# Kernel tuning notes

Measured on AMD Instinct MI355X. Metric: run time of the kernel, lower is better.

The kernel has to match this reference:

```python
import jax, jax.numpy as jnp
import numpy as np

B, T, M, H = 256, 64, 256, 256


def setup_inputs() -> dict:
    key = jax.random.key(0)
    ks = jax.random.split(key, 16)
    n = jax.random.normal
    s = 0.05  # small init so tanh/sigmoid stay in sane range
    return {
        "enc_inputs": n(ks[0], (T, B, M), jnp.float32),  # module transposes (0,1) itself
        "y": n(ks[1], (B, T, 1), jnp.float32),
        "W_d": n(ks[2], (M, 2 * H), jnp.float32) * s,
        "b_Wd": n(ks[3], (M,), jnp.float32) * s,
        "U_d": n(ks[4], (M, M), jnp.float32) * s,
        "v_d": n(ks[5], (1, M), jnp.float32) * s,
        "w_tilda": n(ks[6], (1, M + 1), jnp.float32) * s,
        "b_wt": n(ks[7], (1,), jnp.float32) * s,
        "W_ih": n(ks[8], (4 * H, 1), jnp.float32) * s,
        "W_hh": n(ks[9], (4 * H, H), jnp.float32) * s,
        "b_ih": n(ks[10], (4 * H,), jnp.float32) * s,
        "b_hh": n(ks[11], (4 * H,), jnp.float32) * s,
        "W_y": n(ks[12], (H, H + M), jnp.float32) * s,
        "b_Wy": n(ks[13], (H,), jnp.float32) * s,
        "v_y": n(ks[14], (1, H), jnp.float32) * s,
        "b_vy": n(ks[15], (1,), jnp.float32) * s,
    }


def reference(enc_inputs, y, W_d, b_Wd, U_d, v_d, w_tilda, b_wt,
              W_ih, W_hh, b_ih, b_hh, W_y, b_Wy, v_y, b_vy):
    enc = jnp.swapaxes(enc_inputs, 0, 1)                 # (B,T,M)
    # U_d(enc) is loop-invariant; hoist (same math as recomputing per step)
    y1 = jnp.einsum('btm,nm->btn', enc, U_d)             # (B,T,M)
    ys = jnp.swapaxes(y, 0, 1)                           # (T,B,1) scanned over time
    b = enc.shape[0]
    d0 = jnp.zeros((b, H), enc.dtype)
    s0 = jnp.zeros((b, H), enc.dtype)
    c0 = jnp.zeros((b, M), enc.dtype)

    def step(carry, y_t):
        d, sp, _ = carry
        # Bahdanau-style temporal attention over encoder steps
        x1 = jnp.concatenate([d, sp], axis=1) @ W_d.T + b_Wd      # (B,M)
        l = jnp.tanh(x1[:, None, :] + y1) @ v_d[0]                # (B,T)
        beta = jax.nn.softmax(l, axis=1)
        c = jnp.einsum('bt,btm->bm', beta, enc)                   # (B,M)
        # scalar driving input for the decoder LSTM cell
        y_til = jnp.concatenate([c, y_t], axis=1) @ w_tilda.T + b_wt  # (B,1)
        # torch.nn.LSTMCell update with (h, c) = (d, sp)
        gates = y_til @ W_ih.T + b_ih + d @ W_hh.T + b_hh         # (B,4H)
        i, f, g, o = jnp.split(gates, 4, axis=1)
        sp_new = jax.nn.sigmoid(f) * sp + jax.nn.sigmoid(i) * jnp.tanh(g)
        d_new = jax.nn.sigmoid(o) * jnp.tanh(sp_new)
        return (d_new, sp_new, c), None

    (d, sp, c), _ = jax.lax.scan(step, (d0, s0, c0), ys)
    h = jnp.concatenate([d, c], axis=1) @ W_y.T + b_Wy            # (B,H)
    return h @ v_y.T + b_vy                                        # (B,1)
```

## Files before the change

### kernel.cpp

```cpp
#include <hip/hip_runtime.h>


#define Bx 256
#define Tx 64
#define Mx 256
#define Hx 256
#define NT 1024
#define XS 20

typedef unsigned int  uint;
typedef unsigned short ushort;
typedef _Float16 h2  __attribute__((ext_vector_type(2)));
typedef float    f2v __attribute__((ext_vector_type(2)));

__device__ __forceinline__ float4 ld4(const float* p) { return *(const float4*)p; }
__device__ __forceinline__ float h2f(ushort s) {
  union { ushort s; _Float16 h; } c; c.s = s; return (float)c.h;
}
__device__ __forceinline__ ushort f2h(float f) {
  union { _Float16 h; ushort s; } c; c.h = (_Float16)f; return c.s;
}
__device__ __forceinline__ uint pk2(float a, float b) {
  return (uint)f2h(a) | ((uint)f2h(b) << 16);
}

#if defined(__has_builtin)
#if __has_builtin(__builtin_amdgcn_rcpf)
#define RCPF(x) __builtin_amdgcn_rcpf(x)
#endif
#if __has_builtin(__builtin_amdgcn_fdot2)
#define HAVE_FDOT2 1
#endif
#if __has_builtin(__builtin_amdgcn_cvt_pk_f32_fp8) && __has_builtin(__builtin_amdgcn_cvt_pk_fp8_f32)
#define HAVE_FP8 1
#endif
#endif
#ifndef RCPF
#define RCPF(x) (1.0f / (x))
#endif

__device__ __forceinline__ float tanh_fast(float x) {
  float e2 = __expf(2.0f * x);
  return 1.0f - 2.0f * RCPF(e2 + 1.0f);
}
__device__ __forceinline__ float tanh_pre(float z2) {
  return 1.0f - 2.0f * RCPF(__expf(z2) + 1.0f);
}
__device__ __forceinline__ float sigm(float x) {
  return RCPF(1.0f + __expf(-x));
}
__device__ __forceinline__ float wave_sum(float v) {
  #pragma unroll
  for (int o = 1; o < 64; o <<= 1) v += __shfl_xor(v, o, 64);
  return v;
}
__device__ __forceinline__ int xsw(int m) { return (m >> 4) * XS + (m & 15); }

__device__ __forceinline__ uint sw8(float f) {
  union { float f; uint u; } c; c.f = f;
  uint s = (c.u >> 31) << 7;
  float a = fabsf(f);
  if (!(a >= 0.0009765625f)) return s;
  if (a >= 448.f) return s | 0x7e;
  int e = (int)((c.u >> 23) & 0xff) - 127;
  if (e < -6) { int q = (int)(a * 512.f + 0.5f); return s | (uint)q; }
  uint m = ((c.u & 0x7fffff) + 0x80000) >> 20;
  if (m == 8) { m = 0; ++e; }
  if (e > 8) return s | 0x7e;
  return s | ((uint)(e + 7) << 3) | m;
}
__device__ __forceinline__ float sw8d(uint b) {
  uint s = b >> 7, e = (b >> 3) & 0xf, m = b & 7;
  float v;
  if (e) { union { uint u; float f; } c; c.u = ((e + 120u) << 23) | (m << 20); v = c.f; }
  else v = (float)m * 0.001953125f;
  return s ? -v : v;
}
__device__ __forceinline__ uint pk_fp8x4(float w0, float w1, float w2, float w3) {
#ifdef HAVE_FP8
  int u = 0;
  u = __builtin_amdgcn_cvt_pk_fp8_f32(w0, w1, u, false);
  u = __builtin_amdgcn_cvt_pk_fp8_f32(w2, w3, u, true);
  return (uint)u;
#else
  return sw8(w0) | (sw8(w1) << 8) | (sw8(w2) << 16) | (sw8(w3) << 24);
#endif
}
template <bool HI>
__device__ __forceinline__ f2v dec2(uint w) {
#ifdef HAVE_FP8
  return __builtin_amdgcn_cvt_pk_f32_fp8((int)w, HI);
#else
  uint b0 = HI ? ((w >> 16) & 0xffu) : (w & 0xffu);
  uint b1 = HI ? (w >> 24) : ((w >> 8) & 0xffu);
  return f2v{sw8d(b0), sw8d(b1)};
#endif
}
__device__ __forceinline__ f2v dotq(uint w, float4 a, f2v acc) {
  acc += dec2<false>(w) * f2v{a.x, a.y};
  acc += dec2<true>(w)  * f2v{a.z, a.w};
  return acc;
}

__global__ __launch_bounds__(256)
void pack_weights(const float* __restrict__ W_d,
                  const float* __restrict__ W_hh,
                  const float* __restrict__ U_d,
                  const float* __restrict__ W_y,
                  uint4* __restrict__ Whh8q,
                  uint4* __restrict__ Wd8q,
                  uint4* __restrict__ Ud8,
                  float* __restrict__ Wyt) {
  const int blk = blockIdx.x, tid = threadIdx.x;
  if (blk < 16) {
    const int k16 = blk;
    #pragma unroll
    for (int q = 0; q < 4; ++q) {
      const int j = tid + 256 * q;
      const float* wr = W_hh + (size_t)j * 256 + 16 * k16;
      float4 a = ld4(wr), b = ld4(wr + 4), c = ld4(wr + 8), d = ld4(wr + 12);
      uint4 u;
      u.x = pk_fp8x4(16.f * a.x, 16.f * a.y, 16.f * a.z, 16.f * a.w);
      u.y = pk_fp8x4(16.f * b.x, 16.f * b.y, 16.f * b.z, 16.f * b.w);
      u.z = pk_fp8x4(16.f * c.x, 16.f * c.y, 16.f * c.z, 16.f * c.w);
      u.w = pk_fp8x4(16.f * d.x, 16.f * d.y, 16.f * d.z, 16.f * d.w);
      Whh8q[k16 * 1024 + j] = u;
    }
  } else if (blk < 48) {
    const int k16 = blk - 16;
    const float* wr = W_d + (size_t)tid * 512 + 16 * k16;
    float4 a = ld4(wr), b = ld4(wr + 4), c = ld4(wr + 8), d = ld4(wr + 12);
    uint4 u;
    u.x = pk_fp8x4(16.f * a.x, 16.f * a.y, 16.f * a.z, 16.f * a.w);
    u.y = pk_fp8x4(16.f * b.x, 16.f * b.y, 16.f * b.z, 16.f * b.w);
    u.z = pk_fp8x4(16.f * c.x, 16.f * c.y, 16.f * c.z, 16.f * c.w);
    u.w = pk_fp8x4(16.f * d.x, 16.f * d.y, 16.f * d.z, 16.f * d.w);
    Wd8q[k16 * 256 + tid] = u;
  } else if (blk < 80) {
    const int m8 = blk - 48;
    float4 a = ld4(U_d + (size_t)tid * 256 + 8 * m8);
    float4 b = ld4(U_d + (size_t)tid * 256 + 8 * m8 + 4);
    Ud8[m8 * 256 + tid] = uint4{pk2(2.f * a.x, 2.f * a.y), pk2(2.f * a.z, 2.f * a.w),
                                pk2(2.f * b.x, 2.f * b.y), pk2(2.f * b.z, 2.f * b.w)};
  } else {
    const int k0 = (blk - 80) * 4;
    float4 w = ld4(W_y + (size_t)tid * 512 + k0);
    Wyt[(k0 + 0) * 256 + tid] = w.x;
    Wyt[(k0 + 1) * 256 + tid] = w.y;
    Wyt[(k0 + 2) * 256 + tid] = w.z;
    Wyt[(k0 + 3) * 256 + tid] = w.w;
  }
}

__global__ __launch_bounds__(NT, 1)
void fused(const float* __restrict__ enc,
           const float* __restrict__ yv,
           const float* __restrict__ b_Wd,
           const float* __restrict__ v_d,
           const float* __restrict__ w_tilda,
           const float* __restrict__ b_wt,
           const float* __restrict__ W_ih,
           const float* __restrict__ b_ih,
           const float* __restrict__ b_hh,
           const float* __restrict__ b_Wy,
           const float* __restrict__ v_y,
           const float* __restrict__ b_vy,
           const uint4* __restrict__ Whh8q,
           const uint4* __restrict__ Wd8q,
           const uint4* __restrict__ Ud8,
           const float* __restrict__ Wyt,
           ushort* __restrict__ Y1,
           float* __restrict__ out)
{
  extern __shared__ __align__(16) uint4 dynls[];
  uint4* wdl = dynls;
  uint4* whl = dynls + 8192;
  __shared__ __align__(16) float dsp_s[2 * Hx];
  __shared__ __align__(16) float xq_s[2 * 16 * XS];
  __shared__ __align__(16) float vd_s[16 * XS];
  __shared__ float gates_s[1024];
  __shared__ float dcfin_s[2 * Hx];
  __shared__ float l_s[Tx];
  __shared__ uint  beta2_s[Tx / 2];
  __shared__ float e_s[Tx];
  __shared__ float red_s[4];
  __shared__ float ytil_s;
  __shared__ unsigned flagX, flagL, flagE;

  const int b   = blockIdx.x;
  const int tid = threadIdx.x;
  const int h   = tid & 255;
  const int p   = tid >> 8;
  const size_t BM = (size_t)Bx * Mx;

  #pragma unroll
  for (int i = 0; i < 8; ++i) wdl[i * NT + tid] = Wd8q[i * NT + tid];
  whl[tid] = Whh8q[15 * 1024 + tid];
  if (tid < 256) vd_s[xsw(tid)] = v_d[tid];
  if (tid < 512) dsp_s[tid] = 0.0f;
  if (tid == 0) { flagX = 0u; flagL = 0u; flagE = 0u; }

  float bj0 = 0.f, bj1 = 0.f;
  if (tid < 512) { bj0 = b_ih[tid] + b_hh[tid]; bj1 = b_ih[tid + 512] + b_hh[tid + 512]; }
  float bWd_r = 0.f;
  if (tid >= 512 && tid < 768) bWd_r = 2.0f * b_Wd[tid - 512];
  float wih0 = 0.f, wih1 = 0.f, wih2 = 0.f, wih3 = 0.f;
  if (tid < 256) {
    wih0 = W_ih[tid]; wih1 = W_ih[tid + 256]; wih2 = W_ih[tid + 512]; wih3 = W_ih[tid + 768];
  }
  float yv_r = 0.f;
  if (tid >= 512 && tid < 576) yv_r = yv[b * Tx + (tid - 512)];
  const float wty = w_tilda[Mx];
  const float bwt = b_wt[0];

  if (tid < Tx) {
    const float* er = enc + (size_t)tid * BM + (size_t)b * Mx;
    float acc = 0.0f;
    for (int m = 0; m < Mx; m += 4) {
      float4 e4 = ld4(er + m);
      float4 w4 = ld4(w_tilda + m);
      acc += e4.x * w4.x + e4.y * w4.y + e4.z * w4.z + e4.w * w4.w;
    }
    e_s[tid] = acc;
  }

  {
    const int n = h;
    const float* eb = enc + (size_t)b * Mx;
    for (int tb = p * 16; tb < p * 16 + 16; tb += 8) {
      f2v acc2[8];
      #pragma unroll
      for (int j = 0; j < 8; ++j) acc2[j] = f2v{0.f, 0.f};
      #pragma unroll 2
      for (int m8 = 0; m8 < 32; ++m8) {
        uint4 u = Ud8[m8 * 256 + n];
        f2v w01 = f2v{h2f((ushort)u.x), h2f((ushort)(u.x >> 16))};
        f2v w23 = f2v{h2f((ushort)u.y), h2f((ushort)(u.y >> 16))};
        f2v w45 = f2v{h2f((ushort)u.z), h2f((ushort)(u.z >> 16))};
        f2v w67 = f2v{h2f((ushort)u.w), h2f((ushort)(u.w >> 16))};
        #pragma unroll
        for (int j = 0; j < 8; ++j) {
          const float* ep = eb + (size_t)(tb + j) * BM + 8 * m8;
          float4 ea = ld4(ep), eb4 = ld4(ep + 4);
          acc2[j] += f2v{ea.x, ea.y} * w01;
          acc2[j] += f2v{ea.z, ea.w} * w23;
          acc2[j] += f2v{eb4.x, eb4.y} * w45;
          acc2[j] += f2v{eb4.z, eb4.w} * w67;
        }
      }
      #pragma unroll
      for (int j = 0; j < 8; ++j)
        Y1[((size_t)b * Tx + tb + j) * Mx + n] = f2h(acc2[j].x + acc2[j].y);
    }
  }
  __syncthreads();

  float e_r = 0.0f;
  if (tid >= 512 && tid < 576) e_r = e_s[tid - 512];

  float sp_reg = 0.0f;

  for (int t = 0; t < Tx; ++t) {
    float gi = 0.0f, gg = 0.0f;
    if (tid < 512) {
      f2v ga = f2v{0.f, 0.f}, gb = f2v{0.f, 0.f};
      const uint4* wp = Whh8q + tid;
      #pragma unroll 2
      for (int c = 0; c < 15; ++c) {
        uint4 wa = wp[c * 1024];
        uint4 wb = wp[c * 1024 + 512];
        const float4* ap = (const float4*)dsp_s + 4 * c;
        float4 a0 = ap[0], a1 = ap[1], a2 = ap[2], a3 = ap[3];
        ga = dotq(wa.x, a0, ga); ga = dotq(wa.y, a1, ga);
        ga = dotq(wa.z, a2, ga); ga = dotq(wa.w, a3, ga);
        gb = dotq(wb.x, a0, gb); gb = dotq(wb.y, a1, gb);
        gb = dotq(wb.z, a2, gb); gb = dotq(wb.w, a3, gb);
      }
      {
        uint4 wa = whl[tid];
        uint4 wb = whl[tid + 512];
        const float4* ap = (const float4*)dsp_s + 60;
        float4 a0 = ap[0], a1 = ap[1], a2 = ap[2], a3 = ap[3];
        ga = dotq(wa.x, a0, ga); ga = dotq(wa.y, a1, ga);
        ga = dotq(wa.z, a2, ga); ga = dotq(wa.w, a3, ga);
        gb = dotq(wb.x, a0, gb); gb = dotq(wb.y, a1, gb);
        gb = dotq(wb.z, a2, gb); gb = dotq(wb.w, a3, gb);
      }
      gi = (ga.x + ga.y) * 0.0625f + bj0;
      gg = (gb.x + gb.y) * 0.0625f + bj1;
      if (tid >= 256) {
        gates_s[tid]       = gi;
        gates_s[tid + 512] = gg;
        __threadfence_block();
        if ((tid & 63) == 0)
          __hip_atomic_fetch_add(&flagE, 1u, __ATOMIC_RELEASE, __HIP_MEMORY_SCOPE_WORKGROUP);
      }
    } else {
      const int idx = tid - 512;
      const int m = idx & 255, q = idx >> 8;
      const int tq = idx >> 3, lq = idx & 7;
      const ushort* y1r = Y1 + ((size_t)b * Tx + tq) * Mx + lq * 32;
      uint4 yq0 = *(const uint4*)(y1r);
      uint4 yq1 = *(const uint4*)(y1r + 8);
      uint4 yq2 = *(const uint4*)(y1r + 16);
      uint4 yq3 = *(const uint4*)(y1r + 24);
      {
        f2v xa2 = f2v{0.f, 0.f};
        const uint4* xp = wdl + m + (q * 16) * 256;
        #pragma unroll 4
        for (int i = 0; i < 16; ++i) {
          uint4 u = xp[i * 256];
          const float4* ap = (const float4*)dsp_s + 64 * q + 4 * i;
          float4 a0 = ap[0], a1 = ap[1], a2 = ap[2], a3 = ap[3];
          xa2 = dotq(u.x, a0, xa2); xa2 = dotq(u.y, a1, xa2);
          xa2 = dotq(u.z, a2, xa2); xa2 = dotq(u.w, a3, xa2);
        }
        xq_s[q * (16 * XS) + xsw(m)] = (xa2.x + xa2.y) * 0.125f
                                     + (q == 0 ? bWd_r : 0.0f);
      }
      __threadfence_block();
      if ((threadIdx.x & 63) == 0)
        __hip_atomic_fetch_add(&flagX, 1u, __ATOMIC_RELEASE, __HIP_MEMORY_SCOPE_WORKGROUP);
      const unsigned tgtX = 8u * (unsigned)(t + 1);
      while (__hip_atomic_load(&flagX, __ATOMIC_ACQUIRE, __HIP_MEMORY_SCOPE_WORKGROUP) < tgtX) {}

      {
        float ps = 0.0f;
        uint yy[8] = {yq0.x, yq0.y, yq0.z, yq0.w, yq1.x, yq1.y, yq1.z, yq1.w};
        uint zz[8] = {yq2.x, yq2.y, yq2.z, yq2.w, yq3.x, yq3.y, yq3.z, yq3.w};
        #pragma unroll
        for (int g = 0; g < 8; ++g) {
          const int c   = 2 * lq + (g >> 2);
          const int off = c * XS + 4 * (g & 3);
          float4 xa0 = *(const float4*)(xq_s + off);
          float4 xa1 = *(const float4*)(xq_s + 16 * XS + off);
          float4 vv  = *(const float4*)(vd_s + off);
          uint ya = (g < 4) ? yy[2 * g] : zz[2 * (g - 4)];
          uint yb = (g < 4) ? yy[2 * g + 1] : zz[2 * (g - 4) + 1];
          ps += tanh_pre(xa0.x + xa1.x + h2f((ushort)ya)) * vv.x
              + tanh_pre(xa0.y + xa1.y + h2f((ushort)(ya >> 16))) * vv.y
              + tanh_pre(xa0.z + xa1.z + h2f((ushort)yb)) * vv.z
              + tanh_pre(xa0.w + xa1.w + h2f((ushort)(yb >> 16))) * vv.w;
        }
        ps += __shfl_xor(ps, 1, 64);
        ps += __shfl_xor(ps, 2, 64);
        ps += __shfl_xor(ps, 4, 64);
        if (lq == 0) l_s[tq] = ps;
      }
      __threadfence_block();
      if ((threadIdx.x & 63) == 0)
        __hip_atomic_fetch_add(&flagL, 1u, __ATOMIC_RELEASE, __HIP_MEMORY_SCOPE_WORKGROUP);

      if (idx < 64) {
        __builtin_amdgcn_s_setprio(1);
        const unsigned tgtL = 8u * (unsigned)(t + 1);
        while (__hip_atomic_load(&flagL, __ATOMIC_ACQUIRE, __HIP_MEMORY_SCOPE_WORKGROUP) < tgtL) {}
        float e0  = __expf(l_s[idx]);
        float den = e0;
        float num = e0 * e_r;
        #pragma unroll
        for (int o = 1; o < 64; o <<= 1) {
          den += __shfl_xor(den, o, 64);
          num += __shfl_xor(num, o, 64);
        }
        if (t == Tx - 1) {
          float beta = e0 * RCPF(den);
          float bn = __shfl_xor(beta, 1, 64);
          if (!(idx & 1)) beta2_s[idx >> 1] = pk2(beta, bn);
        }
        if (idx == t) ytil_s = num * RCPF(den) + wty * yv_r + bwt;
        __threadfence_block();
        if (idx == 0)
          __hip_atomic_fetch_add(&flagE, 1u, __ATOMIC_RELEASE, __HIP_MEMORY_SCOPE_WORKGROUP);
        __builtin_amdgcn_s_setprio(0);
      }
    }

    if (tid < 256) {
      const unsigned tgtE = 5u * (unsigned)(t + 1);
      while (__hip_atomic_load(&flagE, __ATOMIC_ACQUIRE, __HIP_MEMORY_SCOPE_WORKGROUP) < tgtE) {}
      __builtin_amdgcn_s_setprio(1);
      const float ytil = ytil_s;
      float fi = sigm(gi                  + ytil * wih0);
      float ff = sigm(gates_s[256 + tid]  + ytil * wih1);
      float fg = tanh_fast(gg             + ytil * wih2);
      float fo = sigm(gates_s[768 + tid]  + ytil * wih3);
      float spn = ff * sp_reg + fi * fg;
      float dn  = fo * tanh_fast(spn);
      sp_reg = spn;
      dsp_s[tid]       = dn;
      dsp_s[256 + tid] = spn;
      if (t == Tx - 1) dcfin_s[tid] = dn;
      __builtin_amdgcn_s_setprio(0);
    }
    __syncthreads();
  }

  if (tid >= 512) {
    const int idx = tid - 512;
    const int m = idx >> 1, q = idx & 1;
    float acc = 0.0f;
    #pragma unroll 4
    for (int j = 0; j < 32; ++j) {
      const int tt = q * 32 + j;
      uint bp = beta2_s[tt >> 1];
      float bb = (tt & 1) ? h2f((ushort)(bp >> 16)) : h2f((ushort)bp);
      acc += bb * enc[(size_t)tt * BM + (size_t)b * Mx + m];
    }
    acc += __shfl_xor(acc, 1, 64);
    if (q == 0) dcfin_s[256 + m] = acc;
  }
  __syncthreads();

  {
    float a = 0.0f;
    const float* wy = Wyt + h;
    for (int k = 128 * p; k < 128 * p + 128; ++k)
      a += wy[(size_t)k * 256] * dcfin_s[k];
    gates_s[p * 256 + h] = a;
  }
  __syncthreads();
  if (tid < 256) {
    float aa = gates_s[h] + gates_s[256 + h] + gates_s[512 + h] + gates_s[768 + h]
             + b_Wy[h];
    float po = aa * v_y[h];
    po = wave_sum(po);
    if ((tid & 63) == 0) red_s[tid >> 6] = po;
  }
  __syncthreads();
  if (tid == 0) out[b] = red_s[0] + red_s[1] + red_s[2] + red_s[3] + b_vy[0];
}

extern "C" void kernel_launch(void* const* d_in, const int* in_sizes, int n_in,
                              void* d_out, int out_size, void* d_ws, size_t ws_size,
                              hipStream_t stream) {
  const float* enc     = (const float*)d_in[0];
  const float* yv      = (const float*)d_in[1];
  const float* W_d     = (const float*)d_in[2];
  const float* b_Wd    = (const float*)d_in[3];
  const float* U_d     = (const float*)d_in[4];
  const float* v_d     = (const float*)d_in[5];
  const float* w_tilda = (const float*)d_in[6];
  const float* b_wt    = (const float*)d_in[7];
  const float* W_ih    = (const float*)d_in[8];
  const float* W_hh    = (const float*)d_in[9];
  const float* b_ih    = (const float*)d_in[10];
  const float* b_hh    = (const float*)d_in[11];
  const float* W_y     = (const float*)d_in[12];
  const float* b_Wy    = (const float*)d_in[13];
  const float* v_y     = (const float*)d_in[14];
  const float* b_vy    = (const float*)d_in[15];
  float* outp = (float*)d_out;

  char* ws = (char*)d_ws;
  uint4* Whh8q = (uint4*)ws;
  uint4* Wd8q  = (uint4*)(ws + (256 << 10));
  uint4* Ud8   = (uint4*)(ws + (384 << 10));
  float* Wyt   = (float*)(ws + (512 << 10));
  ushort* Y1   = (ushort*)(ws + (1024 << 10));

  const int DYN_LDS = (128 + 16) << 10;
  hipFuncSetAttribute((const void*)fused,
                      hipFuncAttributeMaxDynamicSharedMemorySize, DYN_LDS);

  hipLaunchKernelGGL(pack_weights, dim3(208), dim3(256), 0, stream,
                     W_d, W_hh, U_d, W_y, Whh8q, Wd8q, Ud8, Wyt);
  hipLaunchKernelGGL(fused, dim3(Bx), dim3(NT), DYN_LDS, stream,
                     enc, yv, b_Wd, v_d, w_tilda, b_wt, W_ih, b_ih, b_hh,
                     b_Wy, v_y, b_vy, Whh8q, Wd8q, Ud8, Wyt, Y1, outp);
}
```

Measured before the change: 598.2 us.

## Redistribute attention and LSTM gate work across all 1024 threads per step

Each timestep's work is now split across all 16 waves instead of being partitioned into LSTM-gate waves and attention waves. All threads compute the W_d projection, each over an 8-chunk quarter of the input, with four partial sums now stored in xq_s. All threads also compute the tanh/v_d scoring with 16 lanes per time row. Afterwards every thread except the softmax wave computes one W_hh gate row read from global memory, and one wave computes two rows to cover the rows the softmax wave leaves out. The W_hh tail slice is no longer cached in LDS, which shrinks dynamic LDS from 144 KB to 128 KB. The intent is to balance load and shorten the critical path, but the gate computation now runs serially after the attention phase instead of overlapping with it.

```diff
diff --git a/kernel.cpp b/kernel.cpp
--- a/kernel.cpp
+++ b/kernel.cpp
@@ -172,11 +172,9 @@
            ushort* __restrict__ Y1,
            float* __restrict__ out)
 {
-  extern __shared__ __align__(16) uint4 dynls[];
-  uint4* wdl = dynls;
-  uint4* whl = dynls + 8192;
+  extern __shared__ __align__(16) uint4 wdl[];
   __shared__ __align__(16) float dsp_s[2 * Hx];
-  __shared__ __align__(16) float xq_s[2 * 16 * XS];
+  __shared__ __align__(16) float xq_s[4 * 16 * XS];
   __shared__ __align__(16) float vd_s[16 * XS];
   __shared__ float gates_s[1024];
   __shared__ float dcfin_s[2 * Hx];
@@ -191,19 +189,24 @@
   const int tid = threadIdx.x;
   const int h   = tid & 255;
   const int p   = tid >> 8;
+  const int tq  = tid >> 4;
+  const int lq  = tid & 15;
+  const int mq  = tid & 255;
+  const int qq  = tid >> 8;
+  const bool dual = (tid >= 256 && tid < 320);
   const size_t BM = (size_t)Bx * Mx;
 
   #pragma unroll
   for (int i = 0; i < 8; ++i) wdl[i * NT + tid] = Wd8q[i * NT + tid];
-  whl[tid] = Whh8q[15 * 1024 + tid];
   if (tid < 256) vd_s[xsw(tid)] = v_d[tid];
   if (tid < 512) dsp_s[tid] = 0.0f;
   if (tid == 0) { flagX = 0u; flagL = 0u; flagE = 0u; }
 
-  float bj0 = 0.f, bj1 = 0.f;
-  if (tid < 512) { bj0 = b_ih[tid] + b_hh[tid]; bj1 = b_ih[tid + 512] + b_hh[tid + 512]; }
+  float bj0 = b_ih[tid] + b_hh[tid];
+  float bj1 = 0.f;
+  if (dual) bj1 = b_ih[tid + 256] + b_hh[tid + 256];
   float bWd_r = 0.f;
-  if (tid >= 512 && tid < 768) bWd_r = 2.0f * b_Wd[tid - 512];
+  if (tid < 256) bWd_r = 2.0f * b_Wd[tid];
   float wih0 = 0.f, wih1 = 0.f, wih2 = 0.f, wih3 = 0.f;
   if (tid < 256) {
     wih0 = W_ih[tid]; wih1 = W_ih[tid + 256]; wih2 = W_ih[tid + 512]; wih3 = W_ih[tid + 768];
@@ -261,130 +264,119 @@
   float sp_reg = 0.0f;
 
   for (int t = 0; t < Tx; ++t) {
-    float gi = 0.0f, gg = 0.0f;
-    if (tid < 512) {
+    const ushort* y1r = Y1 + ((size_t)b * Tx + tq) * Mx + lq * 16;
+    uint4 yqa = *(const uint4*)(y1r);
+    uint4 yqb = *(const uint4*)(y1r + 8);
+
+    {
+      f2v xa2 = f2v{0.f, 0.f};
+      const uint4* xp = wdl + mq + (qq * 8) * 256;
+      #pragma unroll
+      for (int i = 0; i < 8; ++i) {
+        uint4 u = xp[i * 256];
+        const float4* ap = (const float4*)dsp_s + 4 * (qq * 8 + i);
+        float4 a0 = ap[0], a1 = ap[1], a2 = ap[2], a3 = ap[3];
+        xa2 = dotq(u.x, a0, xa2); xa2 = dotq(u.y, a1, xa2);
+        xa2 = dotq(u.z, a2, xa2); xa2 = dotq(u.w, a3, xa2);
+      }
+      xq_s[qq * (16 * XS) + xsw(mq)] = (xa2.x + xa2.y) * 0.125f
+                                     + (qq == 0 ? bWd_r : 0.0f);
+    }
+    __threadfence_block();
+    if ((tid & 63) == 0)
+      __hip_atomic_fetch_add(&flagX, 1u, __ATOMIC_RELEASE, __HIP_MEMORY_SCOPE_WORKGROUP);
+    const unsigned tgtX = 16u * (unsigned)(t + 1);
+    while (__hip_atomic_load(&flagX, __ATOMIC_ACQUIRE, __HIP_MEMORY_SCOPE_WORKGROUP) < tgtX) {}
+
+    {
+      float ps = 0.0f;
+      uint yy[8] = {yqa.x, yqa.y, yqa.z, yqa.w, yqb.x, yqb.y, yqb.z, yqb.w};
+      #pragma unroll
+      for (int g = 0; g < 4; ++g) {
+        const int off = lq * XS + 4 * g;
+        float4 x0 = *(const float4*)(xq_s + off);
+        float4 x1 = *(const float4*)(xq_s + 320 + off);
+        float4 x2 = *(const float4*)(xq_s + 640 + off);
+        float4 x3 = *(const float4*)(xq_s + 960 + off);
+        float4 vv = *(const float4*)(vd_s + off);
+        uint ya = yy[2 * g], yb = yy[2 * g + 1];
+        ps += tanh_pre(x0.x + x1.x + x2.x + x3.x + h2f((ushort)ya)) * vv.x
+            + tanh_pre(x0.y + x1.y + x2.y + x3.y + h2f((ushort)(ya >> 16))) * vv.y
+            + tanh_pre(x0.z + x1.z + x2.z + x3.z + h2f((ushort)yb)) * vv.z
+            + tanh_pre(x0.w + x1.w + x2.w + x3.w + h2f((ushort)(yb >> 16))) * vv.w;
+      }
+      ps += __shfl_xor(ps, 1, 64);
+      ps += __shfl_xor(ps, 2, 64);
+      ps += __shfl_xor(ps, 4, 64);
+      ps += __shfl_xor(ps, 8, 64);
+      if (lq == 0) l_s[tq] = ps;
+    }
+    __threadfence_block();
+    if ((tid & 63) == 0)
+      __hip_atomic_fetch_add(&flagL, 1u, __ATOMIC_RELEASE, __HIP_MEMORY_SCOPE_WORKGROUP);
+
+    float gi = 0.0f;
+    if (tid >= 512 && tid < 576) {
+      const int idx = tid - 512;
+      __builtin_amdgcn_s_setprio(1);
+      const unsigned tgtL = 16u * (unsigned)(t + 1);
+      while (__hip_atomic_load(&flagL, __ATOMIC_ACQUIRE, __HIP_MEMORY_SCOPE_WORKGROUP) < tgtL) {}
+      float e0  = __expf(l_s[idx]);
+      float den = e0;
+      float num = e0 * e_r;
+      #pragma unroll
+      for (int o = 1; o < 64; o <<= 1) {
+        den += __shfl_xor(den, o, 64);
+        num += __shfl_xor(num, o, 64);
+      }
+      if (t == Tx - 1) {
+        float beta = e0 * RCPF(den);
+        float bn = __shfl_xor(beta, 1, 64);
+        if (!(idx & 1)) beta2_s[idx >> 1] = pk2(beta, bn);
+      }
+      if (idx == t) ytil_s = num * RCPF(den) + wty * yv_r + bwt;
+      __threadfence_block();
+      if (idx == 0)
+        __hip_atomic_fetch_add(&flagE, 1u, __ATOMIC_RELEASE, __HIP_MEMORY_SCOPE_WORKGROUP);
+      __builtin_amdgcn_s_setprio(0);
+    } else {
       f2v ga = f2v{0.f, 0.f}, gb = f2v{0.f, 0.f};
-      const uint4* wp = Whh8q + tid;
+      const uint4* wp  = Whh8q + tid;
+      const uint4* wp2 = Whh8q + tid + 256;
       #pragma unroll 2
-      for (int c = 0; c < 15; ++c) {
-        uint4 wa = wp[c * 1024];
-        uint4 wb = wp[c * 1024 + 512];
+      for (int c = 0; c < 16; ++c) {
+        uint4 u = wp[c * 1024];
         const float4* ap = (const float4*)dsp_s + 4 * c;
         float4 a0 = ap[0], a1 = ap[1], a2 = ap[2], a3 = ap[3];
-        ga = dotq(wa.x, a0, ga); ga = dotq(wa.y, a1, ga);
-        ga = dotq(wa.z, a2, ga); ga = dotq(wa.w, a3, ga);
-        gb = dotq(wb.x, a0, gb); gb = dotq(wb.y, a1, gb);
-        gb = dotq(wb.z, a2, gb); gb = dotq(wb.w, a3, gb);
-      }
-      {
-        uint4 wa = whl[tid];
-        uint4 wb = whl[tid + 512];
-        const float4* ap = (const float4*)dsp_s + 60;
-        float4 a0 = ap[0], a1 = ap[1], a2 = ap[2], a3 = ap[3];
-        ga = dotq(wa.x, a0, ga); ga = dotq(wa.y, a1, ga);
-        ga = dotq(wa.z, a2, ga); ga = dotq(wa.w, a3, ga);
-        gb = dotq(wb.x, a0, gb); gb = dotq(wb.y, a1, gb);
-        gb = dotq(wb.z, a2, gb); gb = dotq(wb.w, a3, gb);
-      }
-      gi = (ga.x + ga.y) * 0.0625f + bj0;
-      gg = (gb.x + gb.y) * 0.0625f + bj1;
-      if (tid >= 256) {
-        gates_s[tid]       = gi;
-        gates_s[tid + 512] = gg;
+        ga = dotq(u.x, a0, ga); ga = dotq(u.y, a1, ga);
+        ga = dotq(u.z, a2, ga); ga = dotq(u.w, a3, ga);
+        if (dual) {
+          uint4 u2 = wp2[c * 1024];
+          gb = dotq(u2.x, a0, gb); gb = dotq(u2.y, a1, gb);
+          gb = dotq(u2.z, a2, gb); gb = dotq(u2.w, a3, gb);
+        }
+      }
+      float giv = (ga.x + ga.y) * 0.0625f + bj0;
+      if (tid < 256) {
+        gi = giv;
+      } else {
+        gates_s[tid] = giv;
+        if (dual) gates_s[tid + 256] = (gb.x + gb.y) * 0.0625f + bj1;
         __threadfence_block();
         if ((tid & 63) == 0)
           __hip_atomic_fetch_add(&flagE, 1u, __ATOMIC_RELEASE, __HIP_MEMORY_SCOPE_WORKGROUP);
       }
-    } else {
-      const int idx = tid - 512;
-      const int m = idx & 255, q = idx >> 8;
-      const int tq = idx >> 3, lq = idx & 7;
-      const ushort* y1r = Y1 + ((size_t)b * Tx + tq) * Mx + lq * 32;
-      uint4 yq0 = *(const uint4*)(y1r);
-      uint4 yq1 = *(const uint4*)(y1r + 8);
-      uint4 yq2 = *(const uint4*)(y1r + 16);
-      uint4 yq3 = *(const uint4*)(y1r + 24);
-      {
-        f2v xa2 = f2v{0.f, 0.f};
-        const uint4* xp = wdl + m + (q * 16) * 256;
-        #pragma unroll 4
-        for (int i = 0; i < 16; ++i) {
-          uint4 u = xp[i * 256];
-          const float4* ap = (const float4*)dsp_s + 64 * q + 4 * i;
-          float4 a0 = ap[0], a1 = ap[1], a2 = ap[2], a3 = ap[3];
-          xa2 = dotq(u.x, a0, xa2); xa2 = dotq(u.y, a1, xa2);
-          xa2 = dotq(u.z, a2, xa2); xa2 = dotq(u.w, a3, xa2);
-        }
-        xq_s[q * (16 * XS) + xsw(m)] = (xa2.x + xa2.y) * 0.125f
-                                     + (q == 0 ? bWd_r : 0.0f);
-      }
-      __threadfence_block();
-      if ((threadIdx.x & 63) == 0)
-        __hip_atomic_fetch_add(&flagX, 1u, __ATOMIC_RELEASE, __HIP_MEMORY_SCOPE_WORKGROUP);
-      const unsigned tgtX = 8u * (unsigned)(t + 1);
-      while (__hip_atomic_load(&flagX, __ATOMIC_ACQUIRE, __HIP_MEMORY_SCOPE_WORKGROUP) < tgtX) {}
-
-      {
-        float ps = 0.0f;
-        uint yy[8] = {yq0.x, yq0.y, yq0.z, yq0.w, yq1.x, yq1.y, yq1.z, yq1.w};
-        uint zz[8] = {yq2.x, yq2.y, yq2.z, yq2.w, yq3.x, yq3.y, yq3.z, yq3.w};
-        #pragma unroll
-        for (int g = 0; g < 8; ++g) {
-          const int c   = 2 * lq + (g >> 2);
-          const int off = c * XS + 4 * (g & 3);
-          float4 xa0 = *(const float4*)(xq_s + off);
-          float4 xa1 = *(const float4*)(xq_s + 16 * XS + off);
-          float4 vv  = *(const float4*)(vd_s + off);
-          uint ya = (g < 4) ? yy[2 * g] : zz[2 * (g - 4)];
-          uint yb = (g < 4) ? yy[2 * g + 1] : zz[2 * (g - 4) + 1];
-          ps += tanh_pre(xa0.x + xa1.x + h2f((ushort)ya)) * vv.x
-              + tanh_pre(xa0.y + xa1.y + h2f((ushort)(ya >> 16))) * vv.y
-              + tanh_pre(xa0.z + xa1.z + h2f((ushort)yb)) * vv.z
-              + tanh_pre(xa0.w + xa1.w + h2f((ushort)(yb >> 16))) * vv.w;
-        }
-        ps += __shfl_xor(ps, 1, 64);
-        ps += __shfl_xor(ps, 2, 64);
-        ps += __shfl_xor(ps, 4, 64);
-        if (lq == 0) l_s[tq] = ps;
-      }
-      __threadfence_block();
-      if ((threadIdx.x & 63) == 0)
-        __hip_atomic_fetch_add(&flagL, 1u, __ATOMIC_RELEASE, __HIP_MEMORY_SCOPE_WORKGROUP);
-
-      if (idx < 64) {
-        __builtin_amdgcn_s_setprio(1);
-        const unsigned tgtL = 8u * (unsigned)(t + 1);
-        while (__hip_atomic_load(&flagL, __ATOMIC_ACQUIRE, __HIP_MEMORY_SCOPE_WORKGROUP) < tgtL) {}
-        float e0  = __expf(l_s[idx]);
-        float den = e0;
-        float num = e0 * e_r;
-        #pragma unroll
-        for (int o = 1; o < 64; o <<= 1) {
-          den += __shfl_xor(den, o, 64);
-          num += __shfl_xor(num, o, 64);
-        }
-        if (t == Tx - 1) {
-          float beta = e0 * RCPF(den);
-          float bn = __shfl_xor(beta, 1, 64);
-          if (!(idx & 1)) beta2_s[idx >> 1] = pk2(beta, bn);
-        }
-        if (idx == t) ytil_s = num * RCPF(den) + wty * yv_r + bwt;
-        __threadfence_block();
-        if (idx == 0)
-          __hip_atomic_fetch_add(&flagE, 1u, __ATOMIC_RELEASE, __HIP_MEMORY_SCOPE_WORKGROUP);
-        __builtin_amdgcn_s_setprio(0);
-      }
     }
 
     if (tid < 256) {
-      const unsigned tgtE = 5u * (unsigned)(t + 1);
+      const unsigned tgtE = 12u * (unsigned)(t + 1);
       while (__hip_atomic_load(&flagE, __ATOMIC_ACQUIRE, __HIP_MEMORY_SCOPE_WORKGROUP) < tgtE) {}
       __builtin_amdgcn_s_setprio(1);
       const float ytil = ytil_s;
-      float fi = sigm(gi                  + ytil * wih0);
-      float ff = sigm(gates_s[256 + tid]  + ytil * wih1);
-      float fg = tanh_fast(gg             + ytil * wih2);
-      float fo = sigm(gates_s[768 + tid]  + ytil * wih3);
+      float fi = sigm(gi                 + ytil * wih0);
+      float ff = sigm(gates_s[256 + tid] + ytil * wih1);
+      float fg = tanh_fast(gates_s[512 + tid] + ytil * wih2);
+      float fo = sigm(gates_s[768 + tid] + ytil * wih3);
       float spn = ff * sp_reg + fi * fg;
       float dn  = fo * tanh_fast(spn);
       sp_reg = spn;
@@ -459,7 +451,7 @@
   float* Wyt   = (float*)(ws + (512 << 10));
   ushort* Y1   = (ushort*)(ws + (1024 << 10));
 
-  const int DYN_LDS = (128 + 16) << 10;
+  const int DYN_LDS = 128 << 10;
   hipFuncSetAttribute((const void*)fused,
                       hipFuncAttributeMaxDynamicSharedMemorySize, DYN_LDS);
 
```

Result: slower. 673.1 us (+12.5%).

## Switch W_hh recurrence to fp16 weights with packed fdot2 on fp16 hidden state

Applied to the files above, without the earlier changes.

Stores W_hh as fp16 instead of scaled fp8 and keeps a half-precision copy of the hidden state in shared memory, so the per-step recurrent matvec uses packed fp16 dot2 instructions instead of fp8 decode plus float FMAs. This removes the per-element fp8 conversion cost and the LDS cache of the last weight chunk. The price is doubled weight bytes read from global/L2 every time step (512 KB instead of 256 KB) and a smaller dynamic LDS allocation, plus reduced precision of the hidden-state operand.

```diff
diff --git a/kernel.cpp b/kernel.cpp
--- a/kernel.cpp
+++ b/kernel.cpp
@@ -55,6 +55,17 @@
   return v;
 }
 __device__ __forceinline__ int xsw(int m) { return (m >> 4) * XS + (m & 15); }
+
+__device__ __forceinline__ float dot2u(uint w, uint a, float acc) {
+#ifdef HAVE_FDOT2
+  h2 W = __builtin_bit_cast(h2, w);
+  h2 A = __builtin_bit_cast(h2, a);
+  return __builtin_amdgcn_fdot2(W, A, acc, false);
+#else
+  return acc + h2f((ushort)w) * h2f((ushort)a)
+             + h2f((ushort)(w >> 16)) * h2f((ushort)(a >> 16));
+#endif
+}
 
 __device__ __forceinline__ uint sw8(float f) {
   union { float f; uint u; } c; c.f = f;
@@ -107,27 +118,24 @@
                   const float* __restrict__ W_hh,
                   const float* __restrict__ U_d,
                   const float* __restrict__ W_y,
-                  uint4* __restrict__ Whh8q,
+                  uint4* __restrict__ WhhH,
                   uint4* __restrict__ Wd8q,
                   uint4* __restrict__ Ud8,
                   float* __restrict__ Wyt) {
   const int blk = blockIdx.x, tid = threadIdx.x;
-  if (blk < 16) {
-    const int k16 = blk;
+  if (blk < 32) {
+    const int c2 = blk;
+    const int base = 16 * (c2 >> 1) + 8 * (c2 & 1);
     #pragma unroll
     for (int q = 0; q < 4; ++q) {
       const int j = tid + 256 * q;
-      const float* wr = W_hh + (size_t)j * 256 + 16 * k16;
-      float4 a = ld4(wr), b = ld4(wr + 4), c = ld4(wr + 8), d = ld4(wr + 12);
-      uint4 u;
-      u.x = pk_fp8x4(16.f * a.x, 16.f * a.y, 16.f * a.z, 16.f * a.w);
-      u.y = pk_fp8x4(16.f * b.x, 16.f * b.y, 16.f * b.z, 16.f * b.w);
-      u.z = pk_fp8x4(16.f * c.x, 16.f * c.y, 16.f * c.z, 16.f * c.w);
-      u.w = pk_fp8x4(16.f * d.x, 16.f * d.y, 16.f * d.z, 16.f * d.w);
-      Whh8q[k16 * 1024 + j] = u;
-    }
-  } else if (blk < 48) {
-    const int k16 = blk - 16;
+      const float* wr = W_hh + (size_t)j * 256 + base;
+      float4 a = ld4(wr), b = ld4(wr + 4);
+      WhhH[c2 * 1024 + j] = uint4{pk2(a.x, a.y), pk2(a.z, a.w),
+                                  pk2(b.x, b.y), pk2(b.z, b.w)};
+    }
+  } else if (blk < 64) {
+    const int k16 = blk - 32;
     const float* wr = W_d + (size_t)tid * 512 + 16 * k16;
     float4 a = ld4(wr), b = ld4(wr + 4), c = ld4(wr + 8), d = ld4(wr + 12);
     uint4 u;
@@ -136,14 +144,14 @@
     u.z = pk_fp8x4(16.f * c.x, 16.f * c.y, 16.f * c.z, 16.f * c.w);
     u.w = pk_fp8x4(16.f * d.x, 16.f * d.y, 16.f * d.z, 16.f * d.w);
     Wd8q[k16 * 256 + tid] = u;
-  } else if (blk < 80) {
-    const int m8 = blk - 48;
+  } else if (blk < 96) {
+    const int m8 = blk - 64;
     float4 a = ld4(U_d + (size_t)tid * 256 + 8 * m8);
     float4 b = ld4(U_d + (size_t)tid * 256 + 8 * m8 + 4);
     Ud8[m8 * 256 + tid] = uint4{pk2(2.f * a.x, 2.f * a.y), pk2(2.f * a.z, 2.f * a.w),
                                 pk2(2.f * b.x, 2.f * b.y), pk2(2.f * b.z, 2.f * b.w)};
   } else {
-    const int k0 = (blk - 80) * 4;
+    const int k0 = (blk - 96) * 4;
     float4 w = ld4(W_y + (size_t)tid * 512 + k0);
     Wyt[(k0 + 0) * 256 + tid] = w.x;
     Wyt[(k0 + 1) * 256 + tid] = w.y;
@@ -165,17 +173,16 @@
            const float* __restrict__ b_Wy,
            const float* __restrict__ v_y,
            const float* __restrict__ b_vy,
-           const uint4* __restrict__ Whh8q,
+           const uint4* __restrict__ WhhH,
            const uint4* __restrict__ Wd8q,
            const uint4* __restrict__ Ud8,
            const float* __restrict__ Wyt,
            ushort* __restrict__ Y1,
            float* __restrict__ out)
 {
-  extern __shared__ __align__(16) uint4 dynls[];
-  uint4* wdl = dynls;
-  uint4* whl = dynls + 8192;
+  extern __shared__ __align__(16) uint4 wdl[];
   __shared__ __align__(16) float dsp_s[2 * Hx];
+  __shared__ __align__(16) ushort dsph_s[Hx];
   __shared__ __align__(16) float xq_s[2 * 16 * XS];
   __shared__ __align__(16) float vd_s[16 * XS];
   __shared__ float gates_s[1024];
@@ -195,9 +202,9 @@
 
   #pragma unroll
   for (int i = 0; i < 8; ++i) wdl[i * NT + tid] = Wd8q[i * NT + tid];
-  whl[tid] = Whh8q[15 * 1024 + tid];
   if (tid < 256) vd_s[xsw(tid)] = v_d[tid];
   if (tid < 512) dsp_s[tid] = 0.0f;
+  if (tid < 256) dsph_s[tid] = 0;
   if (tid == 0) { flagX = 0u; flagL = 0u; flagE = 0u; }
 
   float bj0 = 0.f, bj1 = 0.f;
@@ -263,31 +270,27 @@
   for (int t = 0; t < Tx; ++t) {
     float gi = 0.0f, gg = 0.0f;
     if (tid < 512) {
-      f2v ga = f2v{0.f, 0.f}, gb = f2v{0.f, 0.f};
-      const uint4* wp = Whh8q + tid;
-      #pragma unroll 2
-      for (int c = 0; c < 15; ++c) {
-        uint4 wa = wp[c * 1024];
-        uint4 wb = wp[c * 1024 + 512];
-        const float4* ap = (const float4*)dsp_s + 4 * c;
-        float4 a0 = ap[0], a1 = ap[1], a2 = ap[2], a3 = ap[3];
-        ga = dotq(wa.x, a0, ga); ga = dotq(wa.y, a1, ga);
-        ga = dotq(wa.z, a2, ga); ga = dotq(wa.w, a3, ga);
-        gb = dotq(wb.x, a0, gb); gb = dotq(wb.y, a1, gb);
-        gb = dotq(wb.z, a2, gb); gb = dotq(wb.w, a3, gb);
-      }
-      {
-        uint4 wa = whl[tid];
-        uint4 wb = whl[tid + 512];
-        const float4* ap = (const float4*)dsp_s + 60;
-        float4 a0 = ap[0], a1 = ap[1], a2 = ap[2], a3 = ap[3];
-        ga = dotq(wa.x, a0, ga); ga = dotq(wa.y, a1, ga);
-        ga = dotq(wa.z, a2, ga); ga = dotq(wa.w, a3, ga);
-        gb = dotq(wb.x, a0, gb); gb = dotq(wb.y, a1, gb);
-        gb = dotq(wb.z, a2, gb); gb = dotq(wb.w, a3, gb);
-      }
-      gi = (ga.x + ga.y) * 0.0625f + bj0;
-      gg = (gb.x + gb.y) * 0.0625f + bj1;
+      float ga = 0.0f, gb = 0.0f;
+      const uint4* wp  = WhhH + tid;
+      const uint4* adp = (const uint4*)dsph_s;
+      for (int c = 0; c < 16; ++c) {
+        uint4 a0 = adp[2 * c];
+        uint4 w0 = wp[(2 * c) * 1024];
+        uint4 v0 = wp[(2 * c) * 1024 + 512];
+        ga = dot2u(w0.x, a0.x, ga); ga = dot2u(w0.y, a0.y, ga);
+        ga = dot2u(w0.z, a0.z, ga); ga = dot2u(w0.w, a0.w, ga);
+        gb = dot2u(v0.x, a0.x, gb); gb = dot2u(v0.y, a0.y, gb);
+        gb = dot2u(v0.z, a0.z, gb); gb = dot2u(v0.w, a0.w, gb);
+        uint4 a1 = adp[2 * c + 1];
+        uint4 w1 = wp[(2 * c + 1) * 1024];
+        uint4 v1 = wp[(2 * c + 1) * 1024 + 512];
+        ga = dot2u(w1.x, a1.x, ga); ga = dot2u(w1.y, a1.y, ga);
+        ga = dot2u(w1.z, a1.z, ga); ga = dot2u(w1.w, a1.w, ga);
+        gb = dot2u(v1.x, a1.x, gb); gb = dot2u(v1.y, a1.y, gb);
+        gb = dot2u(v1.z, a1.z, gb); gb = dot2u(v1.w, a1.w, gb);
+      }
+      gi = ga + bj0;
+      gg = gb + bj1;
       if (tid >= 256) {
         gates_s[tid]       = gi;
         gates_s[tid + 512] = gg;
@@ -390,6 +393,7 @@
       sp_reg = spn;
       dsp_s[tid]       = dn;
       dsp_s[256 + tid] = spn;
+      dsph_s[tid]      = f2h(dn);
       if (t == Tx - 1) dcfin_s[tid] = dn;
       __builtin_amdgcn_s_setprio(0);
     }
@@ -453,19 +457,19 @@
   float* outp = (float*)d_out;
 
   char* ws = (char*)d_ws;
-  uint4* Whh8q = (uint4*)ws;
-  uint4* Wd8q  = (uint4*)(ws + (256 << 10));
-  uint4* Ud8   = (uint4*)(ws + (384 << 10));
-  float* Wyt   = (float*)(ws + (512 << 10));
-  ushort* Y1   = (ushort*)(ws + (1024 << 10));
-
-  const int DYN_LDS = (128 + 16) << 10;
+  uint4* WhhH  = (uint4*)ws;
+  uint4* Wd8q  = (uint4*)(ws + (512 << 10));
+  uint4* Ud8   = (uint4*)(ws + (640 << 10));
+  float* Wyt   = (float*)(ws + (768 << 10));
+  ushort* Y1   = (ushort*)(ws + (1280 << 10));
+
+  const int DYN_LDS = 128 << 10;
   hipFuncSetAttribute((const void*)fused,
                       hipFuncAttributeMaxDynamicSharedMemorySize, DYN_LDS);
 
-  hipLaunchKernelGGL(pack_weights, dim3(208), dim3(256), 0, stream,
-                     W_d, W_hh, U_d, W_y, Whh8q, Wd8q, Ud8, Wyt);
+  hipLaunchKernelGGL(pack_weights, dim3(224), dim3(256), 0, stream,
+                     W_d, W_hh, U_d, W_y, WhhH, Wd8q, Ud8, Wyt);
   hipLaunchKernelGGL(fused, dim3(Bx), dim3(NT), DYN_LDS, stream,
                      enc, yv, b_Wd, v_d, w_tilda, b_wt, W_ih, b_ih, b_hh,
-                     b_Wy, v_y, b_vy, Whh8q, Wd8q, Ud8, Wyt, Y1, outp);
-}
+                     b_Wy, v_y, b_vy, WhhH, Wd8q, Ud8, Wyt, Y1, outp);
+}
```

Result: slower. 1.899 ms (+217.5%).
